# Optimization experiments

Hardware: AMD Instinct MI355X
Metric: run time of the kernel (lower is better)

Reference implementation:

```python
import jax
import jax.numpy as jnp
import numpy as np
from jax import lax

B, NS, T, H, V = 4, 96, 8, 256, 32000
L = NS * T
N = NS + 1                    # num_nodes = num_statements + 1 (exit node)
NUM_LAYERS = NS // 16         # avg_statements_per_step = 16 -> 6 execution steps


def _lstm(c, h, x, Wx, Wh, b):
    """flax-style LSTM cell: gates in (i, f, g, o) order."""
    z = x @ Wx + h @ Wh + b
    gi, gf, gg, go = jnp.split(z, 4, axis=-1)
    c2 = jax.nn.sigmoid(gf) * c + jax.nn.sigmoid(gi) * jnp.tanh(gg)
    h2 = jax.nn.sigmoid(go) * jnp.tanh(c2)
    return c2, h2


def _forward(code_statements, code_length, embed, Wx_s, Wh_s, b_s, W_se, b_se,
             Wx_e, Wh_e, b_e, W_hk, b_hk, W_sd, b_sd, W_d1, b_d1, init_a, init_b):
    # ---- statement embedding: LSTM over the T tokens of each statement ----
    tok = embed[code_statements.astype(jnp.int32)]            # [B, L, H]
    tok = jnp.transpose(tok.reshape(B * NS, T, H), (1, 0, 2))  # [T, B*NS, H]
    c0 = jnp.zeros((B * NS, H), tok.dtype)

    def scan_fn(carry, x):
        c, hh = carry
        c, hh = _lstm(c, hh, x, Wx_s, Wh_s, b_s)
        return (c, hh), None

    (_, h_last), _ = lax.scan(scan_fn, (c0, c0), tok)
    stmt = h_last.reshape(B, NS, H)                           # [B, NS, H]

    # ---- skip encoder: pairwise segment-sum embedding for skipping i -> j ----
    node = jnp.concatenate([stmt, jnp.zeros((B, 1, H), stmt.dtype)], axis=1)  # [B,N,H]
    pref = jnp.concatenate(
        [jnp.zeros((B, 1, H), stmt.dtype), jnp.cumsum(node, axis=1)], axis=1)[:, :N]
    skip = (pref[:, None, :, :] - pref[:, :, None, :]) @ W_se + b_se  # [B,N,N,H]

    stmt_len = (code_length // T).astype(jnp.int32)           # exit node index per example

    # ---- execution loop with soft instruction pointer ----
    c = jnp.broadcast_to(init_a, (B, N, H))
    h = jnp.broadcast_to(init_b, (B, N, H))
    p = jnp.zeros((B, N)).at[:, 0].set(1.0)

    def step(c, h, p, skip_nnh, length, layer):
        # per-example: c,h [N,H]; p [N]; skip_nnh [N,N,H]; length scalar
        n = p.shape[0]
        ar = jnp.arange(n)
        if layer == 0:
            mask = jnp.zeros((n, n)).at[:, 1].set(1.0)
        elif layer == NUM_LAYERS - 1:
            mask = jnp.zeros((n, n)).at[:, length].set(1.0)   # force skip to exit
        else:
            mask = 1.0 - jnp.tri(n)                           # strictly forward skips
            mask = jnp.where(ar <= length, mask, 0.0)         # no skips past exit
            mask = mask.at[:, length].set(1.0)                # always allow exit

        # skip attention logits
        skip_keys = skip_nnh @ W_sd + b_sd                    # [N,N,H]
        h_key = h @ W_hk + b_hk                               # [N,H]
        act = jax.nn.relu(jnp.concatenate(
            [jnp.broadcast_to(h_key[:, None, :], (n, n, H)), skip_keys], axis=-1))
        skip_logits = jnp.squeeze(act @ W_d1, -1) + b_d1[0]   # [N,N]
        skip_logits = jnp.where(mask > 0, skip_logits, -jnp.inf)
        skip_p = jax.nn.softmax(skip_logits, axis=-1)

        # one LSTM skip-execution step for every (i, j) pair, vectorized
        z = skip_nnh @ Wx_e + (h @ Wh_e)[:, None, :] + b_e    # [N,N,4H]
        gi, gf, gg, go = jnp.split(z, 4, axis=-1)
        c_prop = jax.nn.sigmoid(gf) * c[:, None, :] + jax.nn.sigmoid(gi) * jnp.tanh(gg)
        h_prop = jax.nn.sigmoid(go) * jnp.tanh(c_prop)
        fwd_edge = (ar[None, :] > ar[:, None])[:, :, None]    # only j > i executes
        c_prop = jnp.where(fwd_edge, c_prop, c[:, None, :])
        h_prop = jnp.where(fwd_edge, h_prop, h[:, None, :])
        valid = (mask[:, :, None] > 0) & (p[:, None, None] > 0)
        c_prop = jnp.where(valid, c_prop, 0.0)
        h_prop = jnp.where(valid, h_prop, 0.0)

        # soft aggregation of proposals weighted by p(i) * skip_p(i -> j)
        w = skip_p * p[:, None]                               # [N,N]
        denom = (w.sum(axis=0) + 1e-7)[:, None]               # [N,1]
        c_new = jnp.einsum('ijh,ij->jh', c_prop, w) / denom
        h_new = jnp.einsum('ijh,ij->jh', h_prop, w) / denom
        p_new = p @ skip_p
        return c_new, h_new, p_new

    for layer in range(NUM_LAYERS):
        c, h, p = jax.vmap(step, in_axes=(0, 0, 0, 0, 0, None))(
            c, h, p, skip, stmt_len, layer)
    return h                                                  # [B, N, H]


def setup_inputs() -> dict:
    key = jax.random.key(0)
    ks = jax.random.split(key, 16)

    def dense(k, fi, fo):
        return jax.random.normal(k, (fi, fo)) * (1.0 / np.sqrt(fi))

    return {
        'code_statements': jax.random.randint(ks[0], (B, L), 0, V, dtype=jnp.int32),
        'code_length': jax.random.randint(ks[1], (B,), 64, L, dtype=jnp.int32),
        'embed': jax.random.normal(ks[2], (V, H)) * 0.02,
        'Wx_s': dense(ks[3], H, 4 * H), 'Wh_s': dense(ks[4], H, 4 * H),
        'b_s': jnp.zeros((4 * H,)),
        'W_se': dense(ks[5], H, H), 'b_se': jnp.zeros((H,)),
        'Wx_e': dense(ks[6], H, 4 * H), 'Wh_e': dense(ks[7], H, 4 * H),
        'b_e': jnp.zeros((4 * H,)),
        'W_hk': dense(ks[8], H, H), 'b_hk': jnp.zeros((H,)),
        'W_sd': dense(ks[9], H, H), 'b_sd': jnp.zeros((H,)),
        'W_d1': dense(ks[10], 2 * H, 1), 'b_d1': jnp.zeros((1,)),
        'init_a': jax.random.normal(ks[11], (H,)),
        'init_b': jax.random.normal(ks[12], (H,)),
    }


def reference(code_statements, code_length, embed, Wx_s, Wh_s, b_s, W_se, b_se,
              Wx_e, Wh_e, b_e, W_hk, b_hk, W_sd, b_sd, W_d1, b_d1, init_a, init_b):
    return _forward(code_statements, code_length, embed, Wx_s, Wh_s, b_s, W_se, b_se,
                    Wx_e, Wh_e, b_e, W_hk, b_hk, W_sd, b_sd, W_d1, b_d1, init_a, init_b)
```

## Files before the change

### kernel.cpp

```cpp
#include <hip/hip_runtime.h>
#include <cstddef>

#define B_   4
#define NS_  96
#define T_   8
#define H_   256
#define N_   97
#define NL_  6
#define R_   388

__device__ __forceinline__ float sigm(float x) {
    return __builtin_amdgcn_rcpf(1.0f + __builtin_amdgcn_exp2f(-1.44269504f * x));
}
__device__ __forceinline__ float tanh_f(float x) {
    return 1.0f - 2.0f * __builtin_amdgcn_rcpf(1.0f + __builtin_amdgcn_exp2f(2.88539008f * x));
}

__device__ __forceinline__ void fma16(float4 a, float4 w0, float4 w1, float4 w2,
                                      float4 w3, float* acc) {
    acc[0] = fmaf(a.x, w0.x, acc[0]); acc[1] = fmaf(a.x, w0.y, acc[1]);
    acc[2] = fmaf(a.x, w0.z, acc[2]); acc[3] = fmaf(a.x, w0.w, acc[3]);
    acc[0] = fmaf(a.y, w1.x, acc[0]); acc[1] = fmaf(a.y, w1.y, acc[1]);
    acc[2] = fmaf(a.y, w1.z, acc[2]); acc[3] = fmaf(a.y, w1.w, acc[3]);
    acc[0] = fmaf(a.z, w2.x, acc[0]); acc[1] = fmaf(a.z, w2.y, acc[1]);
    acc[2] = fmaf(a.z, w2.z, acc[2]); acc[3] = fmaf(a.z, w2.w, acc[3]);
    acc[0] = fmaf(a.w, w3.x, acc[0]); acc[1] = fmaf(a.w, w3.y, acc[1]);
    acc[2] = fmaf(a.w, w3.z, acc[2]); acc[3] = fmaf(a.w, w3.w, acc[3]);
}

__global__ __launch_bounds__(512, 4) void prologue(
        const int* __restrict__ ids, const float* __restrict__ embed,
        const float* __restrict__ Wx_s, const float* __restrict__ b_s,
        const float* __restrict__ b_se, const float* __restrict__ Wx_e,
        const float* __restrict__ b_e, const float* __restrict__ W_sd,
        const float* __restrict__ b_sd, const float* __restrict__ Wh_e,
        const float* __restrict__ init_a, const float* __restrict__ init_b,
        float* __restrict__ xz, float* __restrict__ cz, float* __restrict__ ck,
        float* __restrict__ hw, float* __restrict__ c0, float* __restrict__ h0,
        float* __restrict__ p0) {
    int bid = blockIdx.x, t = threadIdx.x;
    if (bid < 384) {
        __shared__ float As[64][260];
        __shared__ int ridx[64];
        int r0 = (bid >> 3) * 64, n0 = (bid & 7) * 128;
        if (t < 64) ridx[t] = ids[r0 + t];
        __syncthreads();
#pragma unroll
        for (int m = 0; m < 8; m++) {
            int L = m * 512 + t;
            int r = L >> 6, c4 = (L & 63) * 4;
            *(float4*)&As[r][c4] = *(const float4*)(embed + (size_t)ridx[r] * 256 + c4);
        }
        __syncthreads();
        int rg = t >> 5, cg = t & 31;
        float acc[4][4] = {};
        const float* wp = Wx_s + n0 + 4 * cg;
#pragma unroll 4
        for (int kb = 0; kb < 64; kb++) {
            float4 w0 = *(const float4*)(wp + (size_t)(4 * kb + 0) * 1024);
            float4 w1 = *(const float4*)(wp + (size_t)(4 * kb + 1) * 1024);
            float4 w2 = *(const float4*)(wp + (size_t)(4 * kb + 2) * 1024);
            float4 w3 = *(const float4*)(wp + (size_t)(4 * kb + 3) * 1024);
#pragma unroll
            for (int i = 0; i < 4; i++) {
                float4 a = *(const float4*)&As[rg * 4 + i][4 * kb];
                fma16(a, w0, w1, w2, w3, acc[i]);
            }
        }
        int col = n0 + 4 * cg;
        float4 bv = *(const float4*)&b_s[col];
#pragma unroll
        for (int i = 0; i < 4; i++) {
            int r = r0 + rg * 4 + i;
            float4 o = make_float4(acc[i][0] + bv.x, acc[i][1] + bv.y,
                                   acc[i][2] + bv.z, acc[i][3] + bv.w);
            *(float4*)&xz[(size_t)r * 1024 + col] = o;
        }
    } else if (bid < 386) {
        int n = (bid - 384) * 512 + t;
        float acc = b_e[n];
        for (int k = 0; k < 256; k++) acc = fmaf(b_se[k], Wx_e[(size_t)k * 1024 + n], acc);
        cz[n] = acc;
    } else if (bid < 388) {
        int n = (bid - 386) * 512 + t;
        float acc = b_e[n];
        for (int k = 0; k < 256; k++) {
            acc = fmaf(b_se[k], Wx_e[(size_t)k * 1024 + n], acc);
            acc = fmaf(init_b[k], Wh_e[(size_t)k * 1024 + n], acc);
        }
        hw[n] = acc;
    } else if (bid == 388) {
        if (t < 256) {
            float acc = b_sd[t];
            for (int k = 0; k < 256; k++) acc = fmaf(b_se[k], W_sd[(size_t)k * 256 + t], acc);
            ck[t] = acc;
        }
    } else {
        int r0 = (bid - 389) * 8 + (t >> 8) * 4;
        int col = t & 255;
        float ia = init_a[col], ib = init_b[col];
#pragma unroll
        for (int rr = 0; rr < 4; rr++) {
            int row = r0 + rr;
            if (row < R_) {
                c0[(size_t)row * 256 + col] = ia;
                h0[(size_t)row * 256 + col] = ib;
                if (col == 0) p0[row] = ((row % N_) == 0) ? 1.0f : 0.0f;
            }
        }
    }
}

__global__ __launch_bounds__(1024, 4) void lstm_onepass(const float* __restrict__ xz,
        const float* __restrict__ Wh, float* __restrict__ hbuf) {
    __shared__ float zpart[4][4][1024];
    __shared__ float h_s[4][260];
    int t = threadIdx.x;
    int s0 = blockIdx.x * 4;
    int kg = t >> 8, tg = t & 255;
    int sg = t >> 8, cc = t & 255;
    float creg;
    float hreg;
    {
        const float* z0 = xz + ((size_t)(s0 + sg) * T_) * 1024;
        float gi = z0[cc], gg = z0[512 + cc], go = z0[768 + cc];
        creg = sigm(gi) * tanh_f(gg);
        hreg = sigm(go) * tanh_f(creg);
        h_s[sg][cc] = hreg;
    }
    __syncthreads();
    for (int step = 1; step < T_; step++) {
        float4 z[4] = {};
        const float* wp = Wh + (size_t)(kg * 64) * 1024 + 4 * tg;
        int kbase = kg * 64;
#pragma unroll 4
        for (int kb = 0; kb < 16; kb++) {
            float4 w0 = *(const float4*)(wp + (size_t)(4 * kb + 0) * 1024);
            float4 w1 = *(const float4*)(wp + (size_t)(4 * kb + 1) * 1024);
            float4 w2 = *(const float4*)(wp + (size_t)(4 * kb + 2) * 1024);
            float4 w3 = *(const float4*)(wp + (size_t)(4 * kb + 3) * 1024);
            int k = kbase + 4 * kb;
#pragma unroll
            for (int s = 0; s < 4; s++) {
                float4 a = *(const float4*)&h_s[s][k];
                fma16(a, w0, w1, w2, w3, (float*)&z[s]);
            }
        }
#pragma unroll
        for (int s = 0; s < 4; s++)
            *(float4*)&zpart[kg][s][4 * tg] = z[s];
        __syncthreads();
        const float* xzp = xz + ((size_t)(s0 + sg) * T_ + step) * 1024;
        float zv[4];
#pragma unroll
        for (int ga = 0; ga < 4; ga++) {
            int zc = ga * 256 + cc;
            zv[ga] = xzp[zc] + zpart[0][sg][zc] + zpart[1][sg][zc]
                   + zpart[2][sg][zc] + zpart[3][sg][zc];
        }
        creg = sigm(zv[1]) * creg + sigm(zv[0]) * tanh_f(zv[2]);
        hreg = sigm(zv[3]) * tanh_f(creg);
        h_s[sg][cc] = hreg;
        __syncthreads();
    }
    hbuf[(size_t)(s0 + sg) * H_ + cc] = hreg;
}

template<int MT>
__global__ __launch_bounds__(256) void gemm_t(const float* __restrict__ A,
        const float* __restrict__ W, const float* __restrict__ bias,
        const float* __restrict__ subQ, const float* __restrict__ pgate,
        float* __restrict__ C, int R, int NC) {
    __shared__ float As[MT][260];
    __shared__ int anyflag;
    int t = threadIdx.x;
    int n0 = blockIdx.x * 128;
    int r0 = blockIdx.y * MT;
    if (pgate) {
        if (t == 0) anyflag = 0;
        __syncthreads();
        if (t < MT && r0 + t < R && pgate[r0 + t] != 0.0f) anyflag = 1;
        __syncthreads();
        if (!anyflag) return;
    }
#pragma unroll
    for (int m = 0; m < MT / 4; m++) {
        int L = m * 256 + t;
        int r = L >> 6, c4 = (L & 63) * 4;
        int rr = r0 + r;
        float4 v = make_float4(0.f, 0.f, 0.f, 0.f);
        if (rr < R) v = *(const float4*)(A + (size_t)rr * 256 + c4);
        *(float4*)&As[r][c4] = v;
    }
    __syncthreads();
    constexpr int RT = MT / 8;
    int rg = t >> 5, cg = t & 31;
    float acc[RT][4] = {};
    const float* wp = W + n0 + 4 * cg;
#pragma unroll 2
    for (int kb = 0; kb < 64; kb++) {
        float4 w0 = *(const float4*)(wp + (size_t)(4 * kb + 0) * NC);
        float4 w1 = *(const float4*)(wp + (size_t)(4 * kb + 1) * NC);
        float4 w2 = *(const float4*)(wp + (size_t)(4 * kb + 2) * NC);
        float4 w3 = *(const float4*)(wp + (size_t)(4 * kb + 3) * NC);
#pragma unroll
        for (int i = 0; i < RT; i++) {
            float4 a = *(const float4*)&As[rg * RT + i][4 * kb];
            fma16(a, w0, w1, w2, w3, acc[i]);
        }
    }
    int col = n0 + 4 * cg;
    float4 bv = make_float4(0.f, 0.f, 0.f, 0.f);
    if (bias) bv = *(const float4*)&bias[col];
#pragma unroll
    for (int i = 0; i < RT; i++) {
        int r = r0 + rg * RT + i;
        if (r < R) {
            float4 o = make_float4(acc[i][0] + bv.x, acc[i][1] + bv.y,
                                   acc[i][2] + bv.z, acc[i][3] + bv.w);
            if (subQ) {
                float4 s4 = *(const float4*)(subQ + (size_t)r * NC + col);
                o.x -= s4.x; o.y -= s4.y; o.z -= s4.z; o.w -= s4.w;
            }
            *(float4*)&C[(size_t)r * NC + col] = o;
        }
    }
}

__global__ __launch_bounds__(256) void qr_kernel(const float* __restrict__ S,
        const float* __restrict__ Wx_e, const float* __restrict__ W_sd,
        const float* __restrict__ hw, float* __restrict__ q, float* __restrict__ ve0,
        float* __restrict__ r_, float* __restrict__ rT) {
    __shared__ float As[16][260];
    int t = threadIdx.x;
    int bx = blockIdx.x;
    int r0 = blockIdx.y * 16;
#pragma unroll
    for (int m = 0; m < 4; m++) {
        int L = m * 256 + t;
        int r = L >> 6, c4 = (L & 63) * 4;
        int rr = r0 + r;
        float4 v = make_float4(0.f, 0.f, 0.f, 0.f);
        if (rr < R_) v = *(const float4*)(S + (size_t)rr * 256 + c4);
        *(float4*)&As[r][c4] = v;
    }
    __syncthreads();
    bool isq = bx < 8;
    const float* W = isq ? Wx_e : W_sd;
    int NC = isq ? 1024 : 256;
    int n0 = (isq ? bx : bx - 8) * 128;
    int rg = t >> 5, cg = t & 31;
    float acc[2][4] = {};
    const float* wp = W + n0 + 4 * cg;
#pragma unroll 2
    for (int kb = 0; kb < 64; kb++) {
        float4 w0 = *(const float4*)(wp + (size_t)(4 * kb + 0) * NC);
        float4 w1 = *(const float4*)(wp + (size_t)(4 * kb + 1) * NC);
        float4 w2 = *(const float4*)(wp + (size_t)(4 * kb + 2) * NC);
        float4 w3 = *(const float4*)(wp + (size_t)(4 * kb + 3) * NC);
#pragma unroll
        for (int i = 0; i < 2; i++) {
            float4 a = *(const float4*)&As[rg * 2 + i][4 * kb];
            fma16(a, w0, w1, w2, w3, acc[i]);
        }
    }
    int col = n0 + 4 * cg;
#pragma unroll
    for (int i = 0; i < 2; i++) {
        int r = r0 + rg * 2 + i;
        if (r < R_) {
            float4 o = make_float4(acc[i][0], acc[i][1], acc[i][2], acc[i][3]);
            if (isq) {
                *(float4*)&q[(size_t)r * 1024 + col] = o;
                float4 hwv = *(const float4*)&hw[col];
                float4 v0 = make_float4(hwv.x - o.x, hwv.y - o.y, hwv.z - o.z, hwv.w - o.w);
                *(float4*)&ve0[(size_t)r * 1024 + col] = v0;
            } else {
                *(float4*)&r_[(size_t)r * 256 + col] = o;
                int b = r / N_, n = r - b * N_;
                rT[((size_t)b * 256 + col + 0) * 128 + n] = o.x;
                rT[((size_t)b * 256 + col + 1) * 128 + n] = o.y;
                rT[((size_t)b * 256 + col + 2) * 128 + n] = o.z;
                rT[((size_t)b * 256 + col + 3) * 128 + n] = o.w;
            }
        }
    }
}

__global__ __launch_bounds__(1024) void cumsum_k(const float* __restrict__ stmt,
                                                 float* __restrict__ pref) {
    __shared__ float buf[96][256];
    int b = blockIdx.x, t = threadIdx.x;
#pragma unroll
    for (int m = 0; m < 6; m++) {
        int L = m * 1024 + t;
        int r = L >> 6, c4 = (L & 63) * 4;
        *(float4*)&buf[r][c4] = *(const float4*)(stmt + ((size_t)b * NS_ + r) * 256 + c4);
    }
    __syncthreads();
    if (t < 256) {
        float run = 0.0f;
        pref[((size_t)b * N_) * H_ + t] = 0.0f;
        for (int n = 1; n < N_; n++) {
            run += buf[n - 1][t];
            pref[((size_t)b * N_ + n) * H_ + t] = run;
        }
    }
}

__global__ void softmax_once(const float* __restrict__ r, const float* __restrict__ rT,
                             const float* __restrict__ ck, const float* __restrict__ Wd1,
                             const int* __restrict__ code_length,
                             float* __restrict__ spT_mid, float* __restrict__ spT0,
                             float* __restrict__ spT5) {
    __shared__ float ri[H_], ckl[H_], wd[H_];
    __shared__ float part[8][128];
    __shared__ float red[4];
    int t = threadIdx.x;
    int j = t & 127, half = t >> 7;
    int bi = blockIdx.x;
    int b = bi / N_, i = bi % N_;
    if (t < H_) {
        ri[t] = r[(size_t)bi * H_ + t];
        ckl[t] = ck[t];
        wd[t] = Wd1[256 + t];
    }
    __syncthreads();
    int len = code_length[b] / T_;
    bool valid = (j < N_) && ((j > i && j <= len) || (j == len));
    float acc = 0.0f;
    if (valid) {
        const float* rTb = rT + (size_t)b * H_ * 128 + j;
        int h0 = half * 32;
#pragma unroll 4
        for (int hh = 0; hh < 32; hh++) {
            int h = h0 + hh;
            float v = rTb[(size_t)h * 128] - ri[h] + ckl[h];
            acc = fmaf(fmaxf(v, 0.0f), wd[h], acc);
        }
    }
    part[half][j] = acc;
    __syncthreads();
    float logit = -3.0e38f;
    if (t < 128) {
        if (valid)
            logit = part[0][j] + part[1][j] + part[2][j] + part[3][j]
                  + part[4][j] + part[5][j] + part[6][j] + part[7][j];
        float m = logit;
#pragma unroll
        for (int off = 32; off; off >>= 1) m = fmaxf(m, __shfl_xor(m, off));
        if ((t & 63) == 0) red[t >> 6] = m;
    }
    __syncthreads();
    float e = 0.0f;
    if (t < 128) {
        float m = fmaxf(red[0], red[1]);
        e = valid ? __builtin_amdgcn_exp2f(1.44269504f * (logit - m)) : 0.0f;
        float s = e;
#pragma unroll
        for (int off = 32; off; off >>= 1) s += __shfl_xor(s, off);
        if ((t & 63) == 0) red[2 + (t >> 6)] = s;
    }
    __syncthreads();
    if (t < 128 && j < N_) {
        float s = red[2] + red[3];
        size_t o = ((size_t)b * N_ + j) * 128 + i;
        spT_mid[o] = e / s;
        spT0[o] = (j == 1) ? 1.0f : 0.0f;
        spT5[o] = (j == len) ? 1.0f : 0.0f;
    }
}

__global__ __launch_bounds__(512) void aggregate(const float* __restrict__ q,
        const float* __restrict__ ve, const float* __restrict__ spT,
        const float* __restrict__ p, const float* __restrict__ cc,
        const float* __restrict__ hc, float* __restrict__ cn,
        float* __restrict__ hn, float* __restrict__ pn) {
    __shared__ float qj[1024];
    __shared__ float wcol[128];
    __shared__ int vlist[128];
    __shared__ int cnts[2];
    __shared__ float wsums[2];
    __shared__ float parts[2][2][H_];
    int t = threadIdx.x;
    int bj = blockIdx.x;
    int b = bj / N_, j = bj - b * N_;
    bool pred = false;
    int rank = 0;
    if (t < 128) {
        float wv = (t < N_) ? spT[(size_t)bj * 128 + t] * p[b * N_ + t] : 0.f;
        wcol[t] = wv;
        float s = wv;
#pragma unroll
        for (int off = 32; off; off >>= 1) s += __shfl_xor(s, off);
        pred = (wv != 0.0f);
        unsigned long long mask = __ballot(pred);
        int lane = t & 63;
        rank = __popcll(mask & ((1ull << lane) - 1ull));
        if (lane == 0) { cnts[t >> 6] = (int)__popcll(mask); wsums[t >> 6] = s; }
    }
    __syncthreads();
    float wsum = wsums[0] + wsums[1];
    int nv = cnts[0] + cnts[1];
    if (t < 128 && pred) vlist[(t >= 64 ? cnts[0] : 0) + rank] = t;
    if (wsum == 0.0f) {
        if (t < 256) {
            cn[(size_t)bj * H_ + t] = 0.0f;
            hn[(size_t)bj * H_ + t] = 0.0f;
            if (t == 0) pn[bj] = 0.0f;
        }
        return;
    }
    qj[t] = q[(size_t)bj * 1024 + t];
    qj[512 + t] = q[(size_t)bj * 1024 + 512 + t];
    __syncthreads();
    int hh = t & 255, vs = t >> 8;
    float ac = 0.f, ah = 0.f;
    for (int v = vs; v < nv; v += 2) {
        int i = vlist[v];
        float wv = wcol[i];
        size_t rowi = (size_t)b * N_ + i;
        if (j > i) {
            const float* vei = ve + rowi * 1024;
            float gi = qj[hh] + vei[hh];
            float gf = qj[256 + hh] + vei[256 + hh];
            float gg = qj[512 + hh] + vei[512 + hh];
            float go = qj[768 + hh] + vei[768 + hh];
            float c2 = cc[rowi * H_ + hh];
            float cp = sigm(gf) * c2 + sigm(gi) * tanh_f(gg);
            float hp = sigm(go) * tanh_f(cp);
            ac = fmaf(wv, cp, ac);
            ah = fmaf(wv, hp, ah);
        } else {
            ac = fmaf(wv, cc[rowi * H_ + hh], ac);
            ah = fmaf(wv, hc[rowi * H_ + hh], ah);
        }
    }
    parts[vs][0][hh] = ac;
    parts[vs][1][hh] = ah;
    __syncthreads();
    if (t < 256) {
        float inv = __builtin_amdgcn_rcpf(wsum + 1e-7f);
        cn[(size_t)bj * H_ + t] = (parts[0][0][t] + parts[1][0][t]) * inv;
        hn[(size_t)bj * H_ + t] = (parts[0][1][t] + parts[1][1][t]) * inv;
        if (t == 0) pn[bj] = wsum;
    }
}


extern "C" void kernel_launch(void* const* d_in, const int* in_sizes, int n_in,
                              void* d_out, int out_size, void* d_ws, size_t ws_size,
                              hipStream_t stream) {
    const int*   code_statements = (const int*)d_in[0];
    const int*   code_length = (const int*)d_in[1];
    const float* embed = (const float*)d_in[2];
    const float* Wx_s = (const float*)d_in[3];
    const float* Wh_s = (const float*)d_in[4];
    const float* b_s  = (const float*)d_in[5];
    const float* W_se = (const float*)d_in[6];
    const float* b_se = (const float*)d_in[7];
    const float* Wx_e = (const float*)d_in[8];
    const float* Wh_e = (const float*)d_in[9];
    const float* b_e  = (const float*)d_in[10];
    const float* W_sd = (const float*)d_in[13];
    const float* b_sd = (const float*)d_in[14];
    const float* W_d1 = (const float*)d_in[15];
    const float* init_a = (const float*)d_in[17];
    const float* init_b = (const float*)d_in[18];
    float* out = (float*)d_out;

    float* wsf = (float*)d_ws;
    size_t off = 0;
    auto alloc = [&](size_t n) { float* p = wsf + off; off += n; return p; };
    float* cz = alloc(1024);
    float* ck = alloc(256);
    float* hw = alloc(1024);
    float* xz = alloc((size_t)3072 * 1024);
    float* stmt = alloc(384 * 256);
    float* pref = alloc(R_ * 256);
    float* s_   = alloc(R_ * 256);
    float* q  = alloc(R_ * 1024);
    float* r_ = alloc(R_ * 256);
    float* rT = alloc(4 * 256 * 128);
    float* ve = alloc(R_ * 1024);
    float* spT_mid = alloc(R_ * 128);
    float* spT0    = alloc(R_ * 128);
    float* spT5    = alloc(R_ * 128);
    float* p0 = alloc(R_);
    float* p1 = alloc(R_);
    float* c0 = alloc(R_ * 256);
    float* c1 = alloc(R_ * 256);
    float* h0 = alloc(R_ * 256);
    float* h1 = alloc(R_ * 256);

    prologue<<<dim3(438), 512, 0, stream>>>(code_statements, embed, Wx_s, b_s,
                                            b_se, Wx_e, b_e, W_sd, b_sd, Wh_e,
                                            init_a, init_b, xz, cz, ck, hw, c0, h0, p0);
    lstm_onepass<<<dim3(96), 1024, 0, stream>>>(xz, Wh_s, stmt);
    cumsum_k<<<dim3(4), 1024, 0, stream>>>(stmt, pref);
    gemm_t<16><<<dim3(2, 25), 256, 0, stream>>>(pref, W_se, nullptr, nullptr, nullptr,
                                                s_, R_, 256);
    qr_kernel<<<dim3(10, 25), 256, 0, stream>>>(s_, Wx_e, W_sd, hw, q, ve, r_, rT);
    softmax_once<<<dim3(R_), 1024, 0, stream>>>(r_, rT, ck, W_d1, code_length,
                                                spT_mid, spT0, spT5);

    for (int layer = 0; layer < NL_; layer++) {
        bool odd = (layer & 1);
        float* pc = odd ? p1 : p0;
        float* pn = odd ? p0 : p1;
        float* cc = odd ? c1 : c0;
        float* cn = odd ? c0 : c1;
        float* hc = odd ? h1 : h0;
        float* hn = odd ? h0 : h1;
        if (layer == NL_ - 1) hn = out;
        const float* spT = (layer == 0) ? spT0 : (layer == NL_ - 1) ? spT5 : spT_mid;
        aggregate<<<dim3(R_), 512, 0, stream>>>(q, ve, spT, pc, cc, hc, cn, hn, pn);
        if (layer < NL_ - 1)
            gemm_t<16><<<dim3(8, 25), 256, 0, stream>>>(hn, Wh_e, cz, q, pn,
                                                        ve, R_, 1024);
    }
}
```

Measured before the change: 371.5 us.

## Split statement LSTM across more blocks and prefetch weights in GEMM loops

The statement-LSTM kernel now handles 2 sequences per block instead of 4 and launches 192 blocks, so the recurrence is spread over more CUs. In the process, half the threads sit idle during the gate phase and each block reloads Wh. Three GEMM-style loops now register-double-buffer their weight float4 loads by fetching the next k-slice before computing the current one. The aggregate loop hoists the c load and is unrolled by two to expose more memory parallelism.

Result: slower. 415.7 us (+11.9%).

```diff
diff --git a/kernel.cpp b/kernel.cpp
--- a/kernel.cpp
+++ b/kernel.cpp
@@ -55,17 +55,23 @@
         int rg = t >> 5, cg = t & 31;
         float acc[4][4] = {};
         const float* wp = Wx_s + n0 + 4 * cg;
-#pragma unroll 4
+        float4 w0 = *(const float4*)(wp + (size_t)0 * 1024);
+        float4 w1 = *(const float4*)(wp + (size_t)1 * 1024);
+        float4 w2 = *(const float4*)(wp + (size_t)2 * 1024);
+        float4 w3 = *(const float4*)(wp + (size_t)3 * 1024);
+#pragma unroll 2
         for (int kb = 0; kb < 64; kb++) {
-            float4 w0 = *(const float4*)(wp + (size_t)(4 * kb + 0) * 1024);
-            float4 w1 = *(const float4*)(wp + (size_t)(4 * kb + 1) * 1024);
-            float4 w2 = *(const float4*)(wp + (size_t)(4 * kb + 2) * 1024);
-            float4 w3 = *(const float4*)(wp + (size_t)(4 * kb + 3) * 1024);
+            const float* np = wp + (size_t)(kb < 63 ? 4 * kb + 4 : 0) * 1024;
+            float4 nw0 = *(const float4*)(np + (size_t)0 * 1024);
+            float4 nw1 = *(const float4*)(np + (size_t)1 * 1024);
+            float4 nw2 = *(const float4*)(np + (size_t)2 * 1024);
+            float4 nw3 = *(const float4*)(np + (size_t)3 * 1024);
 #pragma unroll
             for (int i = 0; i < 4; i++) {
                 float4 a = *(const float4*)&As[rg * 4 + i][4 * kb];
                 fma16(a, w0, w1, w2, w3, acc[i]);
             }
+            w0 = nw0; w1 = nw1; w2 = nw2; w3 = nw3;
         }
         int col = n0 + 4 * cg;
         float4 bv = *(const float4*)&b_s[col];
@@ -111,17 +117,16 @@
     }
 }
 
-__global__ __launch_bounds__(1024, 4) void lstm_onepass(const float* __restrict__ xz,
+__global__ __launch_bounds__(1024) void lstm_onepass(const float* __restrict__ xz,
         const float* __restrict__ Wh, float* __restrict__ hbuf) {
-    __shared__ float zpart[4][4][1024];
-    __shared__ float h_s[4][260];
+    __shared__ float zpart[4][2][1024];
+    __shared__ float h_s[2][260];
     int t = threadIdx.x;
-    int s0 = blockIdx.x * 4;
+    int s0 = blockIdx.x * 2;
     int kg = t >> 8, tg = t & 255;
-    int sg = t >> 8, cc = t & 255;
-    float creg;
-    float hreg;
-    {
+    int sg = (t >> 8) & 1, cc = t & 255;
+    float creg = 0.0f, hreg = 0.0f;
+    if (t < 512) {
         const float* z0 = xz + ((size_t)(s0 + sg) * T_) * 1024;
         float gi = z0[cc], gg = z0[512 + cc], go = z0[768 + cc];
         creg = sigm(gi) * tanh_f(gg);
@@ -130,7 +135,7 @@
     }
     __syncthreads();
     for (int step = 1; step < T_; step++) {
-        float4 z[4] = {};
+        float4 z[2] = {};
         const float* wp = Wh + (size_t)(kg * 64) * 1024 + 4 * tg;
         int kbase = kg * 64;
 #pragma unroll 4
@@ -141,29 +146,31 @@
             float4 w3 = *(const float4*)(wp + (size_t)(4 * kb + 3) * 1024);
             int k = kbase + 4 * kb;
 #pragma unroll
-            for (int s = 0; s < 4; s++) {
+            for (int s = 0; s < 2; s++) {
                 float4 a = *(const float4*)&h_s[s][k];
                 fma16(a, w0, w1, w2, w3, (float*)&z[s]);
             }
         }
 #pragma unroll
-        for (int s = 0; s < 4; s++)
+        for (int s = 0; s < 2; s++)
             *(float4*)&zpart[kg][s][4 * tg] = z[s];
         __syncthreads();
-        const float* xzp = xz + ((size_t)(s0 + sg) * T_ + step) * 1024;
-        float zv[4];
-#pragma unroll
-        for (int ga = 0; ga < 4; ga++) {
-            int zc = ga * 256 + cc;
-            zv[ga] = xzp[zc] + zpart[0][sg][zc] + zpart[1][sg][zc]
-                   + zpart[2][sg][zc] + zpart[3][sg][zc];
-        }
-        creg = sigm(zv[1]) * creg + sigm(zv[0]) * tanh_f(zv[2]);
-        hreg = sigm(zv[3]) * tanh_f(creg);
-        h_s[sg][cc] = hreg;
+        if (t < 512) {
+            const float* xzp = xz + ((size_t)(s0 + sg) * T_ + step) * 1024;
+            float zv[4];
+#pragma unroll
+            for (int ga = 0; ga < 4; ga++) {
+                int zc = ga * 256 + cc;
+                zv[ga] = xzp[zc] + zpart[0][sg][zc] + zpart[1][sg][zc]
+                       + zpart[2][sg][zc] + zpart[3][sg][zc];
+            }
+            creg = sigm(zv[1]) * creg + sigm(zv[0]) * tanh_f(zv[2]);
+            hreg = sigm(zv[3]) * tanh_f(creg);
+            h_s[sg][cc] = hreg;
+        }
         __syncthreads();
     }
-    hbuf[(size_t)(s0 + sg) * H_ + cc] = hreg;
+    if (t < 512) hbuf[(size_t)(s0 + sg) * H_ + cc] = hreg;
 }
 
 template<int MT>
@@ -197,17 +204,23 @@
     int rg = t >> 5, cg = t & 31;
     float acc[RT][4] = {};
     const float* wp = W + n0 + 4 * cg;
+    float4 w0 = *(const float4*)(wp + (size_t)0 * NC);
+    float4 w1 = *(const float4*)(wp + (size_t)1 * NC);
+    float4 w2 = *(const float4*)(wp + (size_t)2 * NC);
+    float4 w3 = *(const float4*)(wp + (size_t)3 * NC);
 #pragma unroll 2
     for (int kb = 0; kb < 64; kb++) {
-        float4 w0 = *(const float4*)(wp + (size_t)(4 * kb + 0) * NC);
-        float4 w1 = *(const float4*)(wp + (size_t)(4 * kb + 1) * NC);
-        float4 w2 = *(const float4*)(wp + (size_t)(4 * kb + 2) * NC);
-        float4 w3 = *(const float4*)(wp + (size_t)(4 * kb + 3) * NC);
+        const float* np = wp + (size_t)(kb < 63 ? 4 * kb + 4 : 0) * NC;
+        float4 nw0 = *(const float4*)(np + (size_t)0 * NC);
+        float4 nw1 = *(const float4*)(np + (size_t)1 * NC);
+        float4 nw2 = *(const float4*)(np + (size_t)2 * NC);
+        float4 nw3 = *(const float4*)(np + (size_t)3 * NC);
 #pragma unroll
         for (int i = 0; i < RT; i++) {
             float4 a = *(const float4*)&As[rg * RT + i][4 * kb];
             fma16(a, w0, w1, w2, w3, acc[i]);
         }
+        w0 = nw0; w1 = nw1; w2 = nw2; w3 = nw3;
     }
     int col = n0 + 4 * cg;
     float4 bv = make_float4(0.f, 0.f, 0.f, 0.f);
@@ -252,17 +265,23 @@
     int rg = t >> 5, cg = t & 31;
     float acc[2][4] = {};
     const float* wp = W + n0 + 4 * cg;
+    float4 w0 = *(const float4*)(wp + (size_t)0 * NC);
+    float4 w1 = *(const float4*)(wp + (size_t)1 * NC);
+    float4 w2 = *(const float4*)(wp + (size_t)2 * NC);
+    float4 w3 = *(const float4*)(wp + (size_t)3 * NC);
 #pragma unroll 2
     for (int kb = 0; kb < 64; kb++) {
-        float4 w0 = *(const float4*)(wp + (size_t)(4 * kb + 0) * NC);
-        float4 w1 = *(const float4*)(wp + (size_t)(4 * kb + 1) * NC);
-        float4 w2 = *(const float4*)(wp + (size_t)(4 * kb + 2) * NC);
-        float4 w3 = *(const float4*)(wp + (size_t)(4 * kb + 3) * NC);
+        const float* np = wp + (size_t)(kb < 63 ? 4 * kb + 4 : 0) * NC;
+        float4 nw0 = *(const float4*)(np + (size_t)0 * NC);
+        float4 nw1 = *(const float4*)(np + (size_t)1 * NC);
+        float4 nw2 = *(const float4*)(np + (size_t)2 * NC);
+        float4 nw3 = *(const float4*)(np + (size_t)3 * NC);
 #pragma unroll
         for (int i = 0; i < 2; i++) {
             float4 a = *(const float4*)&As[rg * 2 + i][4 * kb];
             fma16(a, w0, w1, w2, w3, acc[i]);
         }
+        w0 = nw0; w1 = nw1; w2 = nw2; w3 = nw3;
     }
     int col = n0 + 4 * cg;
 #pragma unroll
@@ -416,24 +435,27 @@
     __syncthreads();
     int hh = t & 255, vs = t >> 8;
     float ac = 0.f, ah = 0.f;
+#pragma unroll 2
     for (int v = vs; v < nv; v += 2) {
         int i = vlist[v];
         float wv = wcol[i];
         size_t rowi = (size_t)b * N_ + i;
+        float c2 = cc[rowi * H_ + hh];
         if (j > i) {
             const float* vei = ve + rowi * 1024;
-            float gi = qj[hh] + vei[hh];
-            float gf = qj[256 + hh] + vei[256 + hh];
-            float gg = qj[512 + hh] + vei[512 + hh];
-            float go = qj[768 + hh] + vei[768 + hh];
-            float c2 = cc[rowi * H_ + hh];
+            float v0 = vei[hh], v1 = vei[256 + hh], v2 = vei[512 + hh], v3 = vei[768 + hh];
+            float gi = qj[hh] + v0;
+            float gf = qj[256 + hh] + v1;
+            float gg = qj[512 + hh] + v2;
+            float go = qj[768 + hh] + v3;
             float cp = sigm(gf) * c2 + sigm(gi) * tanh_f(gg);
             float hp = sigm(go) * tanh_f(cp);
             ac = fmaf(wv, cp, ac);
             ah = fmaf(wv, hp, ah);
         } else {
-            ac = fmaf(wv, cc[rowi * H_ + hh], ac);
-            ah = fmaf(wv, hc[rowi * H_ + hh], ah);
+            float h2 = hc[rowi * H_ + hh];
+            ac = fmaf(wv, c2, ac);
+            ah = fmaf(wv, h2, ah);
         }
     }
     parts[vs][0][hh] = ac;
@@ -496,7 +518,7 @@
     prologue<<<dim3(438), 512, 0, stream>>>(code_statements, embed, Wx_s, b_s,
                                             b_se, Wx_e, b_e, W_sd, b_sd, Wh_e,
                                             init_a, init_b, xz, cz, ck, hw, c0, h0, p0);
-    lstm_onepass<<<dim3(96), 1024, 0, stream>>>(xz, Wh_s, stmt);
+    lstm_onepass<<<dim3(192), 1024, 0, stream>>>(xz, Wh_s, stmt);
     cumsum_k<<<dim3(4), 1024, 0, stream>>>(stmt, pref);
     gemm_t<16><<<dim3(2, 25), 256, 0, stream>>>(pref, W_se, nullptr, nullptr, nullptr,
                                                 s_, R_, 256);
```
